# Optimization experiments

Hardware: AMD Instinct MI355X
Metric: run time of the kernel (lower is better)

The kernel has to match this reference:

```python
import jax, jax.numpy as jnp
import numpy as np

EMBED_DIM = 1024
LAMBDA_INIT = 0.8
EPS = 1e-5


def setup_inputs() -> dict:
    key = jax.random.key(0)
    ks = jax.random.split(key, 8)
    D = EMBED_DIM
    x = jax.random.normal(ks[0], (4, 2048, D), dtype=jnp.float32)
    # torch Linear weight [out, in]; we store transposed [in, out] for x @ W
    s = 1.0 / np.sqrt(D)
    w_q12 = jax.random.uniform(ks[1], (D, 2 * D), jnp.float32, -s, s)
    w_k12 = jax.random.uniform(ks[2], (D, 2 * D), jnp.float32, -s, s)
    w_v = jax.random.uniform(ks[3], (D, D), jnp.float32, -s, s)
    lambda_q1 = 0.1 * jax.random.normal(ks[4], (D,), jnp.float32)
    lambda_k1 = 0.1 * jax.random.normal(ks[5], (D,), jnp.float32)
    lambda_q2 = 0.1 * jax.random.normal(ks[6], (D,), jnp.float32)
    lambda_k2 = 0.1 * jax.random.normal(ks[7], (D,), jnp.float32)
    return {"x": x, "w_q12": w_q12, "w_k12": w_k12, "w_v": w_v,
            "lambda_q1": lambda_q1, "lambda_k1": lambda_k1,
            "lambda_q2": lambda_q2, "lambda_k2": lambda_k2}


def reference(x, w_q12, w_k12, w_v, lambda_q1, lambda_k1, lambda_q2, lambda_k2):
    D = x.shape[-1]
    scale = D ** (-0.25)
    q12 = jnp.einsum('bsd,de->bse', x, w_q12)
    k12 = jnp.einsum('bsd,de->bse', x, w_k12)
    q1, q2 = jnp.split(q12, 2, axis=-1)
    k1, k2 = jnp.split(k12, 2, axis=-1)
    v = jnp.einsum('bsd,de->bse', x, w_v)
    attn1 = jnp.einsum('bqd,bkd->bqk', q1, k1) * scale
    attn2 = jnp.einsum('bqd,bkd->bqk', q2, k2) * scale
    lam1 = jnp.exp(jnp.sum(lambda_q1 * lambda_k1))
    lam2 = jnp.exp(jnp.sum(lambda_q2 * lambda_k2))
    lam_full = lam1 - lam2 + LAMBDA_INIT
    diff = jax.nn.softmax(attn1, axis=-1) - lam_full * jax.nn.softmax(attn2, axis=-1)
    out = jnp.einsum('bqk,bkd->bqd', diff, v)
    # RMSNorm (no affine), then scale by (1 - lambda_init)
    rms = jnp.sqrt(jnp.mean(out * out, axis=-1, keepdims=True) + EPS)
    return (out / rms) * (1.0 - LAMBDA_INIT)
```

## Files before the change

kernel.cpp:

```cpp
#include <hip/hip_runtime.h>

typedef float f32x4 __attribute__((ext_vector_type(4)));
typedef _Float16 h16x8 __attribute__((ext_vector_type(8)));
typedef _Float16 h16x4 __attribute__((ext_vector_type(4)));

#define GLOAD_LDS16(gp, lp) __builtin_amdgcn_global_load_lds(               \
    (const __attribute__((address_space(1))) void*)(gp),                    \
    (__attribute__((address_space(3))) void*)(lp), 16, 0, 0)

__global__ __launch_bounds__(256) void cast_x(const float* __restrict__ x,
                                              _Float16* __restrict__ xh) {
  long i = (long)blockIdx.x * 256 + threadIdx.x;
  f32x4 a = *(const f32x4*)(x + i * 8);
  f32x4 b = *(const f32x4*)(x + i * 8 + 4);
  h16x8 h;
  h[0] = (_Float16)a[0]; h[1] = (_Float16)a[1];
  h[2] = (_Float16)a[2]; h[3] = (_Float16)a[3];
  h[4] = (_Float16)b[0]; h[5] = (_Float16)b[1];
  h[6] = (_Float16)b[2]; h[7] = (_Float16)b[3];
  *(h16x8*)(xh + i * 8) = h;
}

__global__ __launch_bounds__(256) void tcw(const float* __restrict__ in,
                                           _Float16* __restrict__ out,
                                           int Kd, int Nd, float scale) {
  __shared__ float tile[64][65];
  const int t = threadIdx.x;
  const int k0 = blockIdx.y * 64, n0 = blockIdx.x * 64;
  const int tr = t >> 4, tc = (t & 15) * 4;
#pragma unroll
  for (int i = 0; i < 4; ++i) {
    int r = i * 16 + tr;
    f32x4 a = *(const f32x4*)(in + (long)(k0 + r) * Nd + n0 + tc);
    tile[r][tc + 0] = a[0]; tile[r][tc + 1] = a[1];
    tile[r][tc + 2] = a[2]; tile[r][tc + 3] = a[3];
  }
  __syncthreads();
#pragma unroll
  for (int i = 0; i < 4; ++i) {
    int r = i * 16 + tr;
    h16x4 h;
#pragma unroll
    for (int q = 0; q < 4; ++q) h[q] = (_Float16)(tile[tc + q][r] * scale);
    *(h16x4*)(out + (long)(n0 + r) * Kd + k0 + tc) = h;
  }
}

__global__ __launch_bounds__(256) void trans16(const _Float16* __restrict__ in,
                                               _Float16* __restrict__ out,
                                               int R, int Cd, long ibatch, long obatch) {
  __shared__ _Float16 tile[64][72];
  in += (long)blockIdx.z * ibatch;
  out += (long)blockIdx.z * obatch;
  const int t = threadIdx.x;
  const int r0 = blockIdx.y * 64, c0 = blockIdx.x * 64;
  const int tr = t >> 3, tc8 = (t & 7) * 8;
#pragma unroll
  for (int i = 0; i < 2; ++i) {
    int r = i * 32 + tr;
    h16x8 a = *(const h16x8*)(in + (long)(r0 + r) * Cd + c0 + tc8);
    *(h16x8*)(&tile[r][tc8]) = a;
  }
  __syncthreads();
#pragma unroll
  for (int i = 0; i < 2; ++i) {
    int r = i * 32 + tr;
    h16x8 h;
#pragma unroll
    for (int q = 0; q < 8; ++q) h[q] = tile[tc8 + q][r];
    *(h16x8*)(out + (long)(c0 + r) * R + r0 + tc8) = h;
  }
}

__global__ __launch_bounds__(1024) void lambda_k(const float* __restrict__ lq1,
                                                 const float* __restrict__ lk1,
                                                 const float* __restrict__ lq2,
                                                 const float* __restrict__ lk2,
                                                 float* __restrict__ lam) {
  __shared__ float sh1[16], sh2[16];
  const int t = threadIdx.x;
  float p1 = lq1[t] * lk1[t];
  float p2 = lq2[t] * lk2[t];
#pragma unroll
  for (int off = 1; off < 64; off <<= 1) {
    p1 += __shfl_xor(p1, off);
    p2 += __shfl_xor(p2, off);
  }
  if ((t & 63) == 0) { sh1[t >> 6] = p1; sh2[t >> 6] = p2; }
  __syncthreads();
  if (t == 0) {
    float s1 = 0.f, s2 = 0.f;
    for (int i = 0; i < 16; ++i) { s1 += sh1[i]; s2 += sh2[i]; }
    lam[0] = __expf(s1) - __expf(s2) + 0.8f;
  }
}

template <int NREP, typename CT>
__global__ __launch_bounds__(512, 2) void gemmp(
    const _Float16* __restrict__ A, const _Float16* __restrict__ B,
    CT* __restrict__ C, int K, int lda, int ldb, int ldc,
    long abatch, long bbatch, long cbatch, int nbx, int nby) {
  constexpr int BN = NREP * 64;
  constexpr int L = 2 + NREP / 2;
  __shared__ _Float16 As[4][256 * 32];
  __shared__ _Float16 Bs[4][BN * 32];

  const int nwg = gridDim.x;
  const int orig = blockIdx.x;
  const int qd = nwg >> 3, rm = nwg & 7;
  const int xcd = orig & 7, sub = orig >> 3;
  const int wgid = (xcd < rm ? xcd * (qd + 1) : rm * (qd + 1) + (xcd - rm) * qd) + sub;

  const int bz = wgid / (nbx * nby);
  const int rem = wgid - bz * nbx * nby;
  const int by = rem / nbx;
  const int bx = rem - by * nbx;

  const int t = threadIdx.x;
  const int lane = t & 63, wv = t >> 6;
  const int wm = wv >> 2, wn = wv & 3;
  const int lg = lane >> 4, l15 = lane & 15;

  const _Float16* Ab = A + (long)bz * abatch + (long)(by * 256) * lda;
  const _Float16* Bb = B + (long)bz * bbatch + (long)(bx * BN) * ldb;

  auto stage = [&](int S) {
    const int rg = S & 3;
    const int kof = S * 32;
#pragma unroll
    for (int j = 0; j < 2; ++j) {
      int e = t + j * 512;
      int r = e >> 2, sp = e & 3;
      int gs = (sp - (r >> 1)) & 3;
      GLOAD_LDS16(Ab + (long)r * lda + kof + gs * 8, &As[rg][e * 8]);
    }
#pragma unroll
    for (int j = 0; j < NREP / 2; ++j) {
      int e = t + j * 512;
      int r = e >> 2, sp = e & 3;
      int gs = (sp - (r >> 1)) & 3;
      GLOAD_LDS16(Bb + (long)r * ldb + kof + gs * 8, &Bs[rg][e * 8]);
    }
  };

  f32x4 acc[8][NREP] = {};
  const int NS = K >> 5;

  stage(0); stage(1); stage(2);

  for (int S = 0; S < NS; ++S) {
    if (S + 1 >= NS) {
      asm volatile("s_waitcnt vmcnt(0)" ::: "memory");
    } else if (S + 2 >= NS) {
      if constexpr (NREP == 4) asm volatile("s_waitcnt vmcnt(4)" ::: "memory");
      else                     asm volatile("s_waitcnt vmcnt(3)" ::: "memory");
    } else {
      if constexpr (NREP == 4) asm volatile("s_waitcnt vmcnt(8)" ::: "memory");
      else                     asm volatile("s_waitcnt vmcnt(6)" ::: "memory");
    }
    __builtin_amdgcn_s_barrier();
    asm volatile("" ::: "memory");

    if (S + 3 < NS) stage(S + 3);

    const int rg = S & 3;
    const _Float16* Asb = &As[rg][0];
    const _Float16* Bsb = &Bs[rg][0];
    h16x8 af[8], bf[NREP];
#pragma unroll
    for (int m = 0; m < 8; ++m) {
      int r = wm * 128 + m * 16 + l15;
      int ch = r * 4 + ((lg + (r >> 1)) & 3);
      af[m] = *(const h16x8*)(Asb + ch * 8);
    }
#pragma unroll
    for (int n = 0; n < NREP; ++n) {
      int r = wn * (NREP * 16) + n * 16 + l15;
      int ch = r * 4 + ((lg + (r >> 1)) & 3);
      bf[n] = *(const h16x8*)(Bsb + ch * 8);
    }
    __builtin_amdgcn_s_setprio(1);
#pragma unroll
    for (int m = 0; m < 8; ++m)
#pragma unroll
      for (int n = 0; n < NREP; ++n)
        acc[m][n] = __builtin_amdgcn_mfma_f32_16x16x32_f16(af[m], bf[n], acc[m][n], 0, 0, 0);
    __builtin_amdgcn_s_setprio(0);
  }

  CT* Cb = C + (long)bz * cbatch;
  const int crow0 = by * 256 + wm * 128;
  const int ccol0 = bx * BN + wn * (NREP * 16);
#pragma unroll
  for (int m = 0; m < 8; ++m)
#pragma unroll
    for (int n = 0; n < NREP; ++n)
#pragma unroll
      for (int j = 0; j < 4; ++j)
        Cb[(long)(crow0 + m * 16 + lg * 4 + j) * ldc + ccol0 + n * 16 + l15] =
            (CT)acc[m][n][j];
}

__global__ __launch_bounds__(256) void softmax_diff(const _Float16* __restrict__ S1,
                                                    const _Float16* __restrict__ S2,
                                                    _Float16* __restrict__ D,
                                                    const float* __restrict__ lamp) {
  const long row = (long)blockIdx.x * 4 + (threadIdx.x >> 6);
  const int lane = threadIdx.x & 63;
  const float lam = *lamp;
  const _Float16* s1 = S1 + row * 2048;
  const _Float16* s2 = S2 + row * 2048;
  float v1[32], v2[32];
  float m1 = -3e38f, m2 = -3e38f;
#pragma unroll
  for (int j = 0; j < 4; ++j) {
    h16x8 a = ((const h16x8*)s1)[j * 64 + lane];
    h16x8 b = ((const h16x8*)s2)[j * 64 + lane];
#pragma unroll
    for (int q = 0; q < 8; ++q) {
      v1[j * 8 + q] = (float)a[q]; v2[j * 8 + q] = (float)b[q];
      m1 = fmaxf(m1, v1[j * 8 + q]); m2 = fmaxf(m2, v2[j * 8 + q]);
    }
  }
#pragma unroll
  for (int off = 1; off < 64; off <<= 1) {
    m1 = fmaxf(m1, __shfl_xor(m1, off));
    m2 = fmaxf(m2, __shfl_xor(m2, off));
  }
  float l1 = 0.f, l2 = 0.f;
#pragma unroll
  for (int e = 0; e < 32; ++e) {
    v1[e] = __expf(v1[e] - m1); l1 += v1[e];
    v2[e] = __expf(v2[e] - m2); l2 += v2[e];
  }
#pragma unroll
  for (int off = 1; off < 64; off <<= 1) {
    l1 += __shfl_xor(l1, off);
    l2 += __shfl_xor(l2, off);
  }
  const float r1 = 1.f / l1, r2 = lam / l2;
  _Float16* d = D + row * 2048;
#pragma unroll
  for (int j = 0; j < 4; ++j) {
    h16x8 h;
#pragma unroll
    for (int q = 0; q < 8; ++q)
      h[q] = (_Float16)(v1[j * 8 + q] * r1 - v2[j * 8 + q] * r2);
    ((h16x8*)d)[j * 64 + lane] = h;
  }
}

__global__ __launch_bounds__(256) void rmsnorm(const _Float16* __restrict__ O,
                                               float* __restrict__ out) {
  const long row = (long)blockIdx.x * 4 + (threadIdx.x >> 6);
  const int lane = threadIdx.x & 63;
  const _Float16* o = O + row * 1024;
  h16x8 a = ((const h16x8*)o)[lane];
  h16x8 b = ((const h16x8*)o)[64 + lane];
  float xa[8], xb[8];
  float ss = 0.f;
#pragma unroll
  for (int q = 0; q < 8; ++q) {
    xa[q] = (float)a[q]; xb[q] = (float)b[q];
    ss += xa[q] * xa[q] + xb[q] * xb[q];
  }
#pragma unroll
  for (int off = 1; off < 64; off <<= 1) ss += __shfl_xor(ss, off);
  const float s = 0.2f * rsqrtf(ss * (1.f / 1024.f) + 1e-5f);
  float* po = out + row * 1024;
  f32x4 r;
#pragma unroll
  for (int q = 0; q < 4; ++q) r[q] = xa[q] * s;
  *(f32x4*)(po + lane * 8) = r;
#pragma unroll
  for (int q = 0; q < 4; ++q) r[q] = xa[4 + q] * s;
  *(f32x4*)(po + lane * 8 + 4) = r;
#pragma unroll
  for (int q = 0; q < 4; ++q) r[q] = xb[q] * s;
  *(f32x4*)(po + 512 + lane * 8) = r;
#pragma unroll
  for (int q = 0; q < 4; ++q) r[q] = xb[4 + q] * s;
  *(f32x4*)(po + 512 + lane * 8 + 4) = r;
}

extern "C" void kernel_launch(void* const* d_in, const int* in_sizes, int n_in,
                              void* d_out, int out_size, void* d_ws, size_t ws_size,
                              hipStream_t stream) {
  const float* x   = (const float*)d_in[0];
  const float* wq  = (const float*)d_in[1];
  const float* wk  = (const float*)d_in[2];
  const float* wv  = (const float*)d_in[3];
  const float* lq1 = (const float*)d_in[4];
  const float* lk1 = (const float*)d_in[5];
  const float* lq2 = (const float*)d_in[6];
  const float* lk2 = (const float*)d_in[7];
  float* out = (float*)d_out;

  const size_t MB = 1ull << 20;
  char* ws = (char*)d_ws;
  _Float16* xh   = (_Float16*)(ws + 0);
  _Float16* Wp   = (_Float16*)(ws + 16 * MB);
  _Float16* qkv  = (_Float16*)(ws + 26 * MB);
  _Float16* vt   = (_Float16*)(ws + 106 * MB);
  _Float16* S1   = (_Float16*)(ws + 122 * MB);
  _Float16* S2   = (_Float16*)(ws + 154 * MB);
  float*    lam  = (float*)(ws + 186 * MB);
  _Float16* diff = (_Float16*)(ws + 26 * MB);
  _Float16* opre = (_Float16*)(ws + 58 * MB);

  const float scale = 0.17677669529663689f;

  cast_x<<<4096, 256, 0, stream>>>(x, xh);
  tcw<<<dim3(32, 16), 256, 0, stream>>>(wq, Wp, 1024, 2048, scale);
  tcw<<<dim3(32, 16), 256, 0, stream>>>(wk, Wp + 2048l * 1024, 1024, 2048, 1.0f);
  tcw<<<dim3(16, 16), 256, 0, stream>>>(wv, Wp + 4096l * 1024, 1024, 1024, 1.0f);
  lambda_k<<<1, 1024, 0, stream>>>(lq1, lk1, lq2, lk2, lam);

  gemmp<4, _Float16><<<640, 512, 0, stream>>>(xh, Wp, qkv, 1024, 1024, 1024, 5120,
                                              0, 0, 0, 20, 32);

  trans16<<<dim3(16, 32, 4), 256, 0, stream>>>(qkv + 4096, vt, 2048, 5120,
                                               2048l * 5120, 1024l * 2048);

  gemmp<4, _Float16><<<256, 512, 0, stream>>>(qkv, qkv + 2048, S1, 1024, 5120, 5120, 2048,
                                              2048l * 5120, 2048l * 5120, 2048l * 2048, 8, 8);
  gemmp<4, _Float16><<<256, 512, 0, stream>>>(qkv + 1024, qkv + 3072, S2, 1024, 5120, 5120, 2048,
                                              2048l * 5120, 2048l * 5120, 2048l * 2048, 8, 8);

  softmax_diff<<<2048, 256, 0, stream>>>(S1, S2, diff, lam);

  gemmp<2, _Float16><<<256, 512, 0, stream>>>(diff, vt, opre, 2048, 2048, 2048, 1024,
                                              2048l * 2048, 1024l * 2048, 2048l * 1024, 8, 8);

  rmsnorm<<<2048, 256, 0, stream>>>(opre, out);
}
```

Before: 339.6 us.

## Split GEMM main loop into two interleaved half-phases with precomputed LDS offsets

Restructures the gemmp K-loop into two phases, each loading half of the A fragments, issuing part of the next stage's global-to-LDS prefetch, then running half of the MFMAs. Sched and s_barriers keep the waves in step so memory issue and matrix compute interleave. LDS read offsets and global offsets are precomputed outside the loop, and the full-tile register fragments shrink from 8 to 4 A vectors, which lowers register pressure. The cost is more barriers per iteration and trickier waitcnt accounting, which could stall waves or cause hazards when prefetch timing is off.

```diff
diff --git a/kernel.cpp b/kernel.cpp
--- a/kernel.cpp
+++ b/kernel.cpp
@@ -101,7 +101,6 @@
     CT* __restrict__ C, int K, int lda, int ldb, int ldc,
     long abatch, long bbatch, long cbatch, int nbx, int nby) {
   constexpr int BN = NREP * 64;
-  constexpr int L = 2 + NREP / 2;
   __shared__ _Float16 As[4][256 * 32];
   __shared__ _Float16 Bs[4][BN * 32];
 
@@ -124,68 +123,98 @@
   const _Float16* Ab = A + (long)bz * abatch + (long)(by * 256) * lda;
   const _Float16* Bb = B + (long)bz * bbatch + (long)(bx * BN) * ldb;
 
-  auto stage = [&](int S) {
-    const int rg = S & 3;
-    const int kof = S * 32;
-#pragma unroll
-    for (int j = 0; j < 2; ++j) {
-      int e = t + j * 512;
-      int r = e >> 2, sp = e & 3;
-      int gs = (sp - (r >> 1)) & 3;
-      GLOAD_LDS16(Ab + (long)r * lda + kof + gs * 8, &As[rg][e * 8]);
-    }
-#pragma unroll
-    for (int j = 0; j < NREP / 2; ++j) {
-      int e = t + j * 512;
-      int r = e >> 2, sp = e & 3;
-      int gs = (sp - (r >> 1)) & 3;
-      GLOAD_LDS16(Bb + (long)r * ldb + kof + gs * 8, &Bs[rg][e * 8]);
-    }
-  };
+  const int eA0 = t,       rA0 = eA0 >> 2, sA0 = ((eA0 & 3) - (rA0 >> 1)) & 3;
+  const int eA1 = t + 512, rA1 = eA1 >> 2, sA1 = ((eA1 & 3) - (rA1 >> 1)) & 3;
+  const long goA0 = (long)rA0 * lda + sA0 * 8;
+  const long goA1 = (long)rA1 * lda + sA1 * 8;
+  const int eB0 = t,       rB0 = eB0 >> 2, sB0 = ((eB0 & 3) - (rB0 >> 1)) & 3;
+  const long goB0 = (long)rB0 * ldb + sB0 * 8;
+  const int eB1 = t + 512, rB1 = eB1 >> 2, sB1 = ((eB1 & 3) - (rB1 >> 1)) & 3;
+  const long goB1 = (long)rB1 * ldb + sB1 * 8;
+
+  auto stA0 = [&](int S) { GLOAD_LDS16(Ab + goA0 + S * 32, &As[S & 3][eA0 * 8]); };
+  auto stA1 = [&](int S) { GLOAD_LDS16(Ab + goA1 + S * 32, &As[S & 3][eA1 * 8]); };
+  auto stB0 = [&](int S) { GLOAD_LDS16(Bb + goB0 + S * 32, &Bs[S & 3][eB0 * 8]); };
+  auto stB1 = [&](int S) { GLOAD_LDS16(Bb + goB1 + S * 32, &Bs[S & 3][eB1 * 8]); };
+
+  int offA[8], offB[NREP];
+#pragma unroll
+  for (int m = 0; m < 8; ++m) {
+    int r = wm * 128 + m * 16 + l15;
+    offA[m] = (r * 4 + ((lg + (r >> 1)) & 3)) * 8;
+  }
+#pragma unroll
+  for (int n = 0; n < NREP; ++n) {
+    int r = wn * (NREP * 16) + n * 16 + l15;
+    offB[n] = (r * 4 + ((lg + (r >> 1)) & 3)) * 8;
+  }
 
   f32x4 acc[8][NREP] = {};
   const int NS = K >> 5;
 
-  stage(0); stage(1); stage(2);
+  for (int P = 0; P < 3; ++P) {
+    stA0(P); stA1(P); stB0(P);
+    if constexpr (NREP == 4) stB1(P);
+  }
+  if constexpr (NREP == 4) asm volatile("s_waitcnt vmcnt(8)" ::: "memory");
+  else                     asm volatile("s_waitcnt vmcnt(6)" ::: "memory");
+  __builtin_amdgcn_s_barrier();
 
   for (int S = 0; S < NS; ++S) {
-    if (S + 1 >= NS) {
-      asm volatile("s_waitcnt vmcnt(0)" ::: "memory");
-    } else if (S + 2 >= NS) {
-      if constexpr (NREP == 4) asm volatile("s_waitcnt vmcnt(4)" ::: "memory");
-      else                     asm volatile("s_waitcnt vmcnt(3)" ::: "memory");
-    } else {
-      if constexpr (NREP == 4) asm volatile("s_waitcnt vmcnt(8)" ::: "memory");
-      else                     asm volatile("s_waitcnt vmcnt(6)" ::: "memory");
-    }
-    __builtin_amdgcn_s_barrier();
-    asm volatile("" ::: "memory");
-
-    if (S + 3 < NS) stage(S + 3);
-
     const int rg = S & 3;
     const _Float16* Asb = &As[rg][0];
     const _Float16* Bsb = &Bs[rg][0];
-    h16x8 af[8], bf[NREP];
-#pragma unroll
-    for (int m = 0; m < 8; ++m) {
-      int r = wm * 128 + m * 16 + l15;
-      int ch = r * 4 + ((lg + (r >> 1)) & 3);
-      af[m] = *(const h16x8*)(Asb + ch * 8);
-    }
-#pragma unroll
-    for (int n = 0; n < NREP; ++n) {
-      int r = wn * (NREP * 16) + n * 16 + l15;
-      int ch = r * 4 + ((lg + (r >> 1)) & 3);
-      bf[n] = *(const h16x8*)(Bsb + ch * 8);
-    }
+    const bool pf = (S + 3 < NS);
+    h16x8 af[4], bf[NREP];
+
+#pragma unroll
+    for (int m = 0; m < 4; ++m) af[m] = *(const h16x8*)(Asb + offA[m]);
+#pragma unroll
+    for (int n = 0; n < NREP; ++n) bf[n] = *(const h16x8*)(Bsb + offB[n]);
+    if (pf) { stA0(S + 3); stA1(S + 3); }
+    __builtin_amdgcn_s_barrier();
+    asm volatile("s_waitcnt lgkmcnt(0)" ::: "memory");
+    __builtin_amdgcn_sched_barrier(0);
     __builtin_amdgcn_s_setprio(1);
 #pragma unroll
-    for (int m = 0; m < 8; ++m)
+    for (int m = 0; m < 4; ++m)
 #pragma unroll
       for (int n = 0; n < NREP; ++n)
         acc[m][n] = __builtin_amdgcn_mfma_f32_16x16x32_f16(af[m], bf[n], acc[m][n], 0, 0, 0);
     __builtin_amdgcn_s_setprio(0);
+    __builtin_amdgcn_sched_barrier(0);
+    __builtin_amdgcn_s_barrier();
+
+#pragma unroll
+    for (int m = 0; m < 4; ++m) af[m] = *(const h16x8*)(Asb + offA[4 + m]);
+    if (pf) {
+      stB0(S + 3);
+      if constexpr (NREP == 4) stB1(S + 3);
+    }
+    {
+      const int newer = NS - S - 2;
+      if constexpr (NREP == 4) {
+        if (newer >= 2)      asm volatile("s_waitcnt vmcnt(8)" ::: "memory");
+        else if (newer == 1) asm volatile("s_waitcnt vmcnt(4)" ::: "memory");
+        else                 asm volatile("s_waitcnt vmcnt(0)" ::: "memory");
+      } else {
+        if (newer >= 2)      asm volatile("s_waitcnt vmcnt(6)" ::: "memory");
+        else if (newer == 1) asm volatile("s_waitcnt vmcnt(3)" ::: "memory");
+        else                 asm volatile("s_waitcnt vmcnt(0)" ::: "memory");
+      }
+    }
+    __builtin_amdgcn_s_barrier();
+    asm volatile("s_waitcnt lgkmcnt(0)" ::: "memory");
+    __builtin_amdgcn_sched_barrier(0);
+    __builtin_amdgcn_s_setprio(1);
+#pragma unroll
+    for (int m = 0; m < 4; ++m)
+#pragma unroll
+      for (int n = 0; n < NREP; ++n)
+        acc[4 + m][n] = __builtin_amdgcn_mfma_f32_16x16x32_f16(af[m], bf[n], acc[4 + m][n], 0, 0, 0);
+    __builtin_amdgcn_s_setprio(0);
+    __builtin_amdgcn_sched_barrier(0);
+    __builtin_amdgcn_s_barrier();
   }
 
   CT* Cb = C + (long)bz * cbatch;
```

Measured after the change: 296.5 us. 1.15x faster.
